# Optimization experiments

Measured on AMD Instinct MI355X. Metric: run time of the kernel, lower is better.

## Reference

```python
import jax, jax.numpy as jnp
import numpy as np

N_NODES = 81
N_EDGES = 1620
IN_DIM = 10
HIDDEN = 8192
ACTIONS = 729


def setup_inputs() -> dict:
    key = jax.random.key(0)
    ks = jax.random.split(key, 8)
    x = jax.random.normal(ks[0], (N_NODES, IN_DIM), dtype=jnp.float32)
    edge_index = jax.random.randint(ks[1], (2, N_EDGES), 0, N_NODES, dtype=jnp.int64)
    W_gcn = jax.random.normal(ks[2], (IN_DIM, HIDDEN), dtype=jnp.float32) / np.sqrt(IN_DIM)
    b_gcn = jnp.zeros((HIDDEN,), dtype=jnp.float32)
    ln_g = jnp.ones((HIDDEN,), dtype=jnp.float32)
    ln_b = jnp.zeros((HIDDEN,), dtype=jnp.float32)
    W1 = jax.random.normal(ks[3], (HIDDEN, HIDDEN), dtype=jnp.float32) / np.sqrt(HIDDEN)
    b1 = jnp.zeros((HIDDEN,), dtype=jnp.float32)
    W2 = jax.random.normal(ks[4], (HIDDEN, ACTIONS), dtype=jnp.float32) / np.sqrt(HIDDEN)
    b2 = jnp.zeros((ACTIONS,), dtype=jnp.float32)
    return {"x": x, "edge_index": edge_index, "W_gcn": W_gcn, "b_gcn": b_gcn,
            "ln_g": ln_g, "ln_b": ln_b, "W1": W1, "b1": b1, "W2": W2, "b2": b2}


def _gcn_conv(x, edge_index, W, b):
    # GCNConv with added self-loops and symmetric D^-1/2 (A+I) D^-1/2 normalization
    n = x.shape[0]
    loops = jnp.arange(n, dtype=edge_index.dtype)
    src = jnp.concatenate([edge_index[0], loops])  # [E+N]
    dst = jnp.concatenate([edge_index[1], loops])
    h = x @ W  # [N, H] — transform before propagate, as in PyG
    deg = jnp.zeros((n,), dtype=h.dtype).at[dst].add(1.0)
    dinv = jnp.where(deg > 0, jax.lax.rsqrt(deg), 0.0)
    norm = dinv[src] * dinv[dst]  # [E+N]
    msg = h[src] * norm[:, None]
    out = jnp.zeros_like(h).at[dst].add(msg)
    return out + b


def _layer_norm(h, g, b, eps=1e-5):
    mu = jnp.mean(h, axis=-1, keepdims=True)
    var = jnp.mean(jnp.square(h - mu), axis=-1, keepdims=True)
    return (h - mu) * jax.lax.rsqrt(var + eps) * g + b


def reference(x, edge_index, W_gcn, b_gcn, ln_g, ln_b, W1, b1, W2, b2):
    h = jax.nn.relu(_gcn_conv(x, edge_index, W_gcn, b_gcn))  # [81, H]
    h = _layer_norm(h, ln_g, ln_b)
    # global_add_pool with batch = zeros(81): sum all nodes into one graph row
    g = jnp.sum(h, axis=0, keepdims=True)  # [1, H]
    g = jax.nn.relu(g @ W1 + b1)
    logits = g @ W2 + b2  # [1, ACTIONS]
    return jax.nn.log_softmax(logits, axis=1)
```

## Files before the change

kernel.cpp:

```cpp
#include <hip/hip_runtime.h>
#include <math.h>

#define N_NODES 81
#define N_EDGES 1620
#define IN_DIM 10
#define HIDDEN 8192
#define ACTIONS 729
#define KCH 256

__global__ __launch_bounds__(256) void stats_kernel(const float* __restrict__ x,
                                                    const int* __restrict__ ei,
                                                    const float* __restrict__ Wg,
                                                    const float* __restrict__ bg,
                                                    float* __restrict__ yr_all,
                                                    float* __restrict__ stats,
                                                    float* __restrict__ logits,
                                                    unsigned* __restrict__ counter) {
    const int n = blockIdx.x;
    const int t = threadIdx.x;
    __shared__ float deg[N_NODES];
    __shared__ float yr[IN_DIM];
    __shared__ float red[8];

    if (t < N_NODES) deg[t] = 1.0f;
    if (t < IN_DIM) yr[t] = 0.0f;
    __syncthreads();
    for (int e = t; e < N_EDGES; e += 256) atomicAdd(&deg[ei[N_EDGES + e]], 1.0f);
    __syncthreads();
    if (t < N_NODES) deg[t] = rsqrtf(deg[t]);
    __syncthreads();
    const float dn = deg[n];
    for (int e = t; e < N_EDGES; e += 256) {
        if (ei[N_EDGES + e] == n) {
            int s = ei[e];
            float nrm = deg[s] * dn;
            #pragma unroll
            for (int c = 0; c < IN_DIM; ++c) atomicAdd(&yr[c], nrm * x[s * IN_DIM + c]);
        }
    }
    if (t == 0) {
        float nrm = dn * dn;
        #pragma unroll
        for (int c = 0; c < IN_DIM; ++c) atomicAdd(&yr[c], nrm * x[n * IN_DIM + c]);
    }
    __syncthreads();
    if (t < IN_DIM) yr_all[n * IN_DIM + t] = yr[t];
    if (n == 0) {
        for (int a = t; a < ACTIONS; a += 256) logits[a] = 0.f;
        if (t == 0) *counter = 0u;
    }

    const float4* Wg4 = (const float4*)Wg;
    const float4* bg4 = (const float4*)bg;
    float s = 0.f, s2 = 0.f;
    #pragma unroll
    for (int k = 0; k < 8; ++k) {
        int j4 = t + k * 256;
        float4 h = bg4[j4];
        #pragma unroll
        for (int c = 0; c < IN_DIM; ++c) {
            float4 w = Wg4[c * (HIDDEN / 4) + j4];
            float yc = yr[c];
            h.x = fmaf(yc, w.x, h.x);
            h.y = fmaf(yc, w.y, h.y);
            h.z = fmaf(yc, w.z, h.z);
            h.w = fmaf(yc, w.w, h.w);
        }
        h.x = fmaxf(h.x, 0.f); h.y = fmaxf(h.y, 0.f);
        h.z = fmaxf(h.z, 0.f); h.w = fmaxf(h.w, 0.f);
        s  += h.x + h.y + h.z + h.w;
        s2 += h.x * h.x + h.y * h.y + h.z * h.z + h.w * h.w;
    }
    #pragma unroll
    for (int off = 32; off > 0; off >>= 1) { s += __shfl_xor(s, off); s2 += __shfl_xor(s2, off); }
    int wave = t >> 6, lane = t & 63;
    if (lane == 0) { red[wave] = s; red[4 + wave] = s2; }
    __syncthreads();
    if (t == 0) {
        float S  = red[0] + red[1] + red[2] + red[3];
        float S2 = red[4] + red[5] + red[6] + red[7];
        float mu = S * (1.f / HIDDEN);
        float var = S2 * (1.f / HIDDEN) - mu * mu;
        stats[2 * n]     = mu;
        stats[2 * n + 1] = rsqrtf(var + 1e-5f);
    }
}

__global__ __launch_bounds__(256) void gemv1_kernel(const float* __restrict__ Wg,
                                                    const float* __restrict__ bg,
                                                    const float* __restrict__ lng,
                                                    const float* __restrict__ lnb,
                                                    const float* __restrict__ yr_all,
                                                    const float* __restrict__ stats,
                                                    const float* __restrict__ W1,
                                                    float* __restrict__ partial) {
    const int ct = blockIdx.x;
    const int ch = blockIdx.y;
    const int row0 = ch * 32;
    const int t = threadIdx.x;

    __shared__ float syr[N_NODES * IN_DIM];
    __shared__ float sstat[2 * N_NODES];
    __shared__ float sw[IN_DIM][32];
    __shared__ float gred[8][32];
    __shared__ float gl[32];

    for (int i = t; i < N_NODES * IN_DIM; i += 256) syr[i] = yr_all[i];
    for (int i = t; i < 2 * N_NODES; i += 256) sstat[i] = stats[i];
    if (t < 32) {
        #pragma unroll
        for (int c = 0; c < IN_DIM; ++c) sw[c][t] = Wg[c * HIDDEN + row0 + t];
    }
    __syncthreads();

    {
        const int r = t & 31, grp = t >> 5;
        const float bgv = bg[row0 + r];
        float acc = 0.f;
        for (int n = grp; n < N_NODES; n += 8) {
            float h = bgv;
            #pragma unroll
            for (int c = 0; c < IN_DIM; ++c) h = fmaf(syr[n * IN_DIM + c], sw[c][r], h);
            h = fmaxf(h, 0.f);
            acc += (h - sstat[2 * n]) * sstat[2 * n + 1];
        }
        gred[grp][r] = acc;
    }
    __syncthreads();
    if (t < 32) {
        float a = 0.f;
        #pragma unroll
        for (int gq = 0; gq < 8; ++gq) a += gred[gq][t];
        gl[t] = a * lng[row0 + t] + (float)N_NODES * lnb[row0 + t];
    }
    __syncthreads();

    float4 acc = make_float4(0.f, 0.f, 0.f, 0.f);
    const float4* p = (const float4*)(W1 + (size_t)row0 * HIDDEN + ct * 1024) + t;
    #pragma unroll 8
    for (int i = 0; i < 32; ++i) {
        float4 w = p[(size_t)i * (HIDDEN / 4)];
        float gi = gl[i];
        acc.x = fmaf(gi, w.x, acc.x);
        acc.y = fmaf(gi, w.y, acc.y);
        acc.z = fmaf(gi, w.z, acc.z);
        acc.w = fmaf(gi, w.w, acc.w);
    }
    ((float4*)(partial + (size_t)ch * HIDDEN + ct * 1024))[t] = acc;
}

__global__ __launch_bounds__(256) void gemv2_lsm_kernel(const float* __restrict__ partial,
                                                        const float* __restrict__ b1,
                                                        const float* __restrict__ W2,
                                                        const float* __restrict__ b2,
                                                        float* __restrict__ logits,
                                                        unsigned* __restrict__ counter,
                                                        float* __restrict__ out) {
    const int ch = blockIdx.x;
    const int row0 = ch * 32;
    const int t = threadIdx.x;
    __shared__ float sred[8][32];
    __shared__ float gl[32];
    __shared__ int isLast;

    {
        const int r = t & 31, grp = t >> 5;
        float a = 0.f;
        #pragma unroll 4
        for (int c = grp; c < KCH; c += 8) a += partial[(size_t)c * HIDDEN + row0 + r];
        sred[grp][r] = a;
    }
    __syncthreads();
    if (t < 32) {
        float S = b1[row0 + t];
        #pragma unroll
        for (int gq = 0; gq < 8; ++gq) S += sred[gq][t];
        gl[t] = fmaxf(S, 0.f);
    }
    __syncthreads();

    float s0 = 0.f, s1 = 0.f, s2v = 0.f;
    const bool has2 = (t + 512) < ACTIONS;
    #pragma unroll 4
    for (int i = 0; i < 32; ++i) {
        float gi = gl[i];
        const float* r = W2 + (size_t)(row0 + i) * ACTIONS;
        s0 = fmaf(gi, r[t], s0);
        s1 = fmaf(gi, r[t + 256], s1);
        if (has2) s2v = fmaf(gi, r[t + 512], s2v);
    }
    atomicAdd(&logits[t], s0);
    atomicAdd(&logits[t + 256], s1);
    if (has2) atomicAdd(&logits[t + 512], s2v);

    asm volatile("s_waitcnt vmcnt(0)" ::: "memory");
    __syncthreads();
    if (t == 0) isLast = (atomicAdd(counter, 1u) == 255u) ? 1 : 0;
    __syncthreads();

    if (isLast) {
        float l0 = __hip_atomic_load(&logits[t], __ATOMIC_RELAXED,
                                     __HIP_MEMORY_SCOPE_AGENT) + b2[t];
        float l1 = __hip_atomic_load(&logits[t + 256], __ATOMIC_RELAXED,
                                     __HIP_MEMORY_SCOPE_AGENT) + b2[t + 256];
        float l2 = has2 ? (__hip_atomic_load(&logits[t + 512], __ATOMIC_RELAXED,
                                             __HIP_MEMORY_SCOPE_AGENT) + b2[t + 512])
                        : -INFINITY;
        float m = fmaxf(fmaxf(l0, l1), l2);
        #pragma unroll
        for (int off = 32; off > 0; off >>= 1) m = fmaxf(m, __shfl_xor(m, off));
        if ((t & 63) == 0) sred[0][t >> 6] = m;
        __syncthreads();
        float M = fmaxf(fmaxf(sred[0][0], sred[0][1]), fmaxf(sred[0][2], sred[0][3]));
        __syncthreads();
        float e = __expf(l0 - M) + __expf(l1 - M) + (has2 ? __expf(l2 - M) : 0.f);
        #pragma unroll
        for (int off = 32; off > 0; off >>= 1) e += __shfl_xor(e, off);
        if ((t & 63) == 0) sred[0][t >> 6] = e;
        __syncthreads();
        float Se = sred[0][0] + sred[0][1] + sred[0][2] + sred[0][3];
        float L = logf(Se);
        out[t] = l0 - M - L;
        out[t + 256] = l1 - M - L;
        if (has2) out[t + 512] = l2 - M - L;
    }
}

extern "C" void kernel_launch(void* const* d_in, const int* in_sizes, int n_in,
                              void* d_out, int out_size, void* d_ws, size_t ws_size,
                              hipStream_t stream) {
    const float* x    = (const float*)d_in[0];
    const int*   ei   = (const int*)  d_in[1];
    const float* Wg   = (const float*)d_in[2];
    const float* bg   = (const float*)d_in[3];
    const float* lng  = (const float*)d_in[4];
    const float* lnb  = (const float*)d_in[5];
    const float* W1   = (const float*)d_in[6];
    const float* b1   = (const float*)d_in[7];
    const float* W2   = (const float*)d_in[8];
    const float* b2   = (const float*)d_in[9];
    float* out = (float*)d_out;

    float* ws = (float*)d_ws;
    float* logits    = ws;
    unsigned* counter = (unsigned*)(ws + 1024);
    float* stats   = ws + 1088;
    float* yr_all  = ws + 1280;
    float* partial = ws + 4096;

    stats_kernel<<<N_NODES, 256, 0, stream>>>(x, ei, Wg, bg, yr_all, stats, logits, counter);
    gemv1_kernel<<<dim3(8, KCH), 256, 0, stream>>>(Wg, bg, lng, lnb, yr_all, stats, W1, partial);
    gemv2_lsm_kernel<<<256, 256, 0, stream>>>(partial, b1, W2, b2, logits, counter, out);
}
```

Before: 95.98 us.

## Make each gemv1 block cover full W1 rows and template the K-chunk count

The first GEMV kernel now gives each block a slab of R full rows of W1, either 16 or 32 chosen by workspace size. Before, a block handled a 32-row by 1024-column tile on a 2D grid. Each thread keeps 8 float4 accumulators across the whole 8192-wide row, so the small GCN/LayerNorm recomputation is done once per row chunk instead of 8 times, and more loads are in flight per thread. The cost is more partial-sum rows for the second kernel to reduce (512 instead of 256 when the workspace allows it) and higher register pressure.

```diff
diff --git a/kernel.cpp b/kernel.cpp
--- a/kernel.cpp
+++ b/kernel.cpp
@@ -6,7 +6,6 @@
 #define IN_DIM 10
 #define HIDDEN 8192
 #define ACTIONS 729
-#define KCH 256
 
 __global__ __launch_bounds__(256) void stats_kernel(const float* __restrict__ x,
                                                     const int* __restrict__ ei,
@@ -86,6 +85,7 @@
     }
 }
 
+template<int R>
 __global__ __launch_bounds__(256) void gemv1_kernel(const float* __restrict__ Wg,
                                                     const float* __restrict__ bg,
                                                     const float* __restrict__ lng,
@@ -94,61 +94,69 @@
                                                     const float* __restrict__ stats,
                                                     const float* __restrict__ W1,
                                                     float* __restrict__ partial) {
-    const int ct = blockIdx.x;
-    const int ch = blockIdx.y;
-    const int row0 = ch * 32;
+    const int ch = blockIdx.x;
+    const int row0 = ch * R;
     const int t = threadIdx.x;
+    constexpr int NGRP = 256 / R;
 
     __shared__ float syr[N_NODES * IN_DIM];
     __shared__ float sstat[2 * N_NODES];
-    __shared__ float sw[IN_DIM][32];
-    __shared__ float gred[8][32];
-    __shared__ float gl[32];
+    __shared__ float sw[IN_DIM * R];
+    __shared__ float gred[256];
+    __shared__ float gl[R];
 
     for (int i = t; i < N_NODES * IN_DIM; i += 256) syr[i] = yr_all[i];
     for (int i = t; i < 2 * N_NODES; i += 256) sstat[i] = stats[i];
-    if (t < 32) {
-        #pragma unroll
-        for (int c = 0; c < IN_DIM; ++c) sw[c][t] = Wg[c * HIDDEN + row0 + t];
+    if (t < R) {
+        #pragma unroll
+        for (int c = 0; c < IN_DIM; ++c) sw[c * R + t] = Wg[c * HIDDEN + row0 + t];
     }
     __syncthreads();
 
     {
-        const int r = t & 31, grp = t >> 5;
+        const int r = t % R, grp = t / R;
         const float bgv = bg[row0 + r];
         float acc = 0.f;
-        for (int n = grp; n < N_NODES; n += 8) {
+        for (int n = grp; n < N_NODES; n += NGRP) {
             float h = bgv;
             #pragma unroll
-            for (int c = 0; c < IN_DIM; ++c) h = fmaf(syr[n * IN_DIM + c], sw[c][r], h);
+            for (int c = 0; c < IN_DIM; ++c) h = fmaf(syr[n * IN_DIM + c], sw[c * R + r], h);
             h = fmaxf(h, 0.f);
             acc += (h - sstat[2 * n]) * sstat[2 * n + 1];
         }
-        gred[grp][r] = acc;
-    }
-    __syncthreads();
-    if (t < 32) {
+        gred[t] = acc;
+    }
+    __syncthreads();
+    if (t < R) {
         float a = 0.f;
         #pragma unroll
-        for (int gq = 0; gq < 8; ++gq) a += gred[gq][t];
+        for (int gq = 0; gq < NGRP; ++gq) a += gred[gq * R + t];
         gl[t] = a * lng[row0 + t] + (float)N_NODES * lnb[row0 + t];
     }
     __syncthreads();
 
-    float4 acc = make_float4(0.f, 0.f, 0.f, 0.f);
-    const float4* p = (const float4*)(W1 + (size_t)row0 * HIDDEN + ct * 1024) + t;
-    #pragma unroll 8
-    for (int i = 0; i < 32; ++i) {
-        float4 w = p[(size_t)i * (HIDDEN / 4)];
-        float gi = gl[i];
-        acc.x = fmaf(gi, w.x, acc.x);
-        acc.y = fmaf(gi, w.y, acc.y);
-        acc.z = fmaf(gi, w.z, acc.z);
-        acc.w = fmaf(gi, w.w, acc.w);
-    }
-    ((float4*)(partial + (size_t)ch * HIDDEN + ct * 1024))[t] = acc;
-}
-
+    float4 acc[8];
+    #pragma unroll
+    for (int k = 0; k < 8; ++k) acc[k] = make_float4(0.f, 0.f, 0.f, 0.f);
+    const float4* p = (const float4*)W1 + (size_t)row0 * (HIDDEN / 4) + t;
+    #pragma unroll 2
+    for (int r = 0; r < R; ++r) {
+        float gi = gl[r];
+        #pragma unroll
+        for (int k = 0; k < 8; ++k) {
+            float4 w = p[r * (HIDDEN / 4) + k * 256];
+            acc[k].x = fmaf(gi, w.x, acc[k].x);
+            acc[k].y = fmaf(gi, w.y, acc[k].y);
+            acc[k].z = fmaf(gi, w.z, acc[k].z);
+            acc[k].w = fmaf(gi, w.w, acc[k].w);
+        }
+    }
+    float4* q = (float4*)partial + (size_t)ch * (HIDDEN / 4) + t;
+    #pragma unroll
+    for (int k = 0; k < 8; ++k) q[k * 256] = acc[k];
+}
+
+template<int KCH>
 __global__ __launch_bounds__(256) void gemv2_lsm_kernel(const float* __restrict__ partial,
                                                         const float* __restrict__ b1,
                                                         const float* __restrict__ W2,
@@ -249,6 +257,13 @@
     float* partial = ws + 4096;
 
     stats_kernel<<<N_NODES, 256, 0, stream>>>(x, ei, Wg, bg, yr_all, stats, logits, counter);
-    gemv1_kernel<<<dim3(8, KCH), 256, 0, stream>>>(Wg, bg, lng, lnb, yr_all, stats, W1, partial);
-    gemv2_lsm_kernel<<<256, 256, 0, stream>>>(partial, b1, W2, b2, logits, counter, out);
-}
+
+    const size_t need512 = (4096 + (size_t)512 * HIDDEN) * sizeof(float);
+    if (ws_size >= need512) {
+        gemv1_kernel<16><<<512, 256, 0, stream>>>(Wg, bg, lng, lnb, yr_all, stats, W1, partial);
+        gemv2_lsm_kernel<512><<<256, 256, 0, stream>>>(partial, b1, W2, b2, logits, counter, out);
+    } else {
+        gemv1_kernel<32><<<256, 256, 0, stream>>>(Wg, bg, lng, lnb, yr_all, stats, W1, partial);
+        gemv2_lsm_kernel<256><<<256, 256, 0, stream>>>(partial, b1, W2, b2, logits, counter, out);
+    }
+}
```

New measurement: 104.7 us. +9.1%, slower.
